# Performance work log

Hardware: AMD Instinct MI355X
Metric: run time of the kernel (lower is better)

## Reference

```python
import jax, jax.numpy as jnp
import numpy as np

N_NODES = 100000
N_EDGES = 600000
D_FEAT = 128
N_OUT = 1


def setup_inputs() -> dict:
    key = jax.random.key(0)
    k1, k2, k3, k4 = jax.random.split(key, 4)
    node_inputs = jax.random.normal(k1, (N_NODES, D_FEAT), dtype=jnp.float32)
    r_indices = jax.random.randint(k2, (N_EDGES,), 0, N_NODES, dtype=jnp.int64)
    c_indices = jax.random.randint(k3, (N_EDGES,), 0, N_NODES, dtype=jnp.int64)
    w = jax.random.normal(k4, (D_FEAT, N_OUT), dtype=jnp.float32) * 0.05
    b = jnp.zeros((N_OUT,), dtype=jnp.float32)
    return {"node_inputs": node_inputs, "r_indices": r_indices,
            "c_indices": c_indices, "w": w, "b": b}


def reference(node_inputs, r_indices, c_indices, w, b):
    # Gather edge endpoints: [E, D]
    row_inputs = node_inputs[r_indices]
    col_inputs = node_inputs[c_indices]
    diff = jnp.abs(row_inputs - col_inputs)          # [E, D]
    out = diff @ w + b                               # [E, n_out]
    out = jnp.squeeze(out, axis=-1)                  # n_out == 1
    return out  # act is identity (default)
```

## Files before the change

### kernel.cpp

```cpp
#include <hip/hip_runtime.h>
#include <hip/hip_bf16.h>


#define D_FEAT 128

__global__ __launch_bounds__(256) void mlp_decoder_edge_kernel(
    const float* __restrict__ nodes,
    const int*   __restrict__ r_idx,
    const int*   __restrict__ c_idx,
    const float* __restrict__ w,
    const float* __restrict__ b,
    float*       __restrict__ out,
    int n_edges)
{
    const int tid  = blockIdx.x * blockDim.x + threadIdx.x;
    const int lane = tid & 31;
    const int edge = tid >> 5;
    if (edge >= n_edges) return;

    const int r = r_idx[edge];
    const int c = c_idx[edge];

    const float4 wv = ((const float4*)w)[lane];

    const float4 av = ((const float4*)(nodes + (size_t)r * D_FEAT))[lane];
    const float4 bv = ((const float4*)(nodes + (size_t)c * D_FEAT))[lane];

    float s = fabsf(av.x - bv.x) * wv.x
            + fabsf(av.y - bv.y) * wv.y
            + fabsf(av.z - bv.z) * wv.z
            + fabsf(av.w - bv.w) * wv.w;

    #pragma unroll
    for (int off = 16; off > 0; off >>= 1)
        s += __shfl_xor(s, off, 64);

    if (lane == 0)
        out[edge] = s + b[0];
}

extern "C" void kernel_launch(void* const* d_in, const int* in_sizes, int n_in,
                              void* d_out, int out_size, void* d_ws, size_t ws_size,
                              hipStream_t stream) {
    const float* nodes = (const float*)d_in[0];
    const int*   r_idx = (const int*)d_in[1];
    const int*   c_idx = (const int*)d_in[2];
    const float* w     = (const float*)d_in[3];
    const float* b     = (const float*)d_in[4];
    float*       out   = (float*)d_out;

    const int n_edges = in_sizes[1];
    const int threads_needed = n_edges * 32;
    const int block = 256;
    const int grid  = (threads_needed + block - 1) / block;

    mlp_decoder_edge_kernel<<<grid, block, 0, stream>>>(
        nodes, r_idx, c_idx, w, b, out, n_edges);
}
```

Before: 159.6 us.

## Convert node table to fp16 in a pre-pass and gather half-precision rows

Adds a kernel that converts the fp32 node feature table into an fp16 copy in workspace on every call. A new edge kernel then gathers fp16 rows using 16 lanes per edge, eight features per lane, accumulating in fp32. The aim is to halve the bytes moved by the random row gathers, which dominate the cost. In exchange it pays for an extra full-table read and write plus a second launch, and rounding inputs to fp16 adds error. The original fp32 path is kept as a fallback when the workspace is too small.

```diff
diff --git a/kernel.cpp b/kernel.cpp
--- a/kernel.cpp
+++ b/kernel.cpp
@@ -1,10 +1,74 @@
 #include <hip/hip_runtime.h>
 #include <hip/hip_bf16.h>
+#include <hip/hip_fp16.h>
 
 
 #define D_FEAT 128
 
-__global__ __launch_bounds__(256) void mlp_decoder_edge_kernel(
+__global__ __launch_bounds__(256) void convert_f32_to_f16(
+    const float* __restrict__ src, __half* __restrict__ dst, int n8)
+{
+    const int i = blockIdx.x * blockDim.x + threadIdx.x;
+    if (i >= n8) return;
+    const float4* s = (const float4*)src + 2 * (size_t)i;
+    const float4 a = s[0];
+    const float4 c = s[1];
+    float4 packed;
+    ((__half2*)&packed)[0] = __floats2half2_rn(a.x, a.y);
+    ((__half2*)&packed)[1] = __floats2half2_rn(a.z, a.w);
+    ((__half2*)&packed)[2] = __floats2half2_rn(c.x, c.y);
+    ((__half2*)&packed)[3] = __floats2half2_rn(c.z, c.w);
+    ((float4*)dst)[i] = packed;
+}
+
+__global__ __launch_bounds__(256) void gather_edges_f16(
+    const __half* __restrict__ tbl,
+    const int*   __restrict__ r_idx,
+    const int*   __restrict__ c_idx,
+    const float* __restrict__ w,
+    const float* __restrict__ b,
+    float*       __restrict__ out,
+    int n_edges)
+{
+    const int tid  = blockIdx.x * blockDim.x + threadIdx.x;
+    const int lane = tid & 15;
+    const int edge = tid >> 4;
+    if (edge >= n_edges) return;
+
+    const int r = r_idx[edge];
+    const int c = c_idx[edge];
+
+    const float4 w0 = ((const float4*)w)[2 * lane + 0];
+    const float4 w1 = ((const float4*)w)[2 * lane + 1];
+
+    const float4 araw = ((const float4*)(tbl + (size_t)r * D_FEAT))[lane];
+    const float4 braw = ((const float4*)(tbl + (size_t)c * D_FEAT))[lane];
+    const __half2* ah = (const __half2*)&araw;
+    const __half2* bh = (const __half2*)&braw;
+
+    const float2 a0 = __half22float2(ah[0]), b0 = __half22float2(bh[0]);
+    const float2 a1 = __half22float2(ah[1]), b1 = __half22float2(bh[1]);
+    const float2 a2 = __half22float2(ah[2]), b2 = __half22float2(bh[2]);
+    const float2 a3 = __half22float2(ah[3]), b3 = __half22float2(bh[3]);
+
+    float s = fabsf(a0.x - b0.x) * w0.x
+            + fabsf(a0.y - b0.y) * w0.y
+            + fabsf(a1.x - b1.x) * w0.z
+            + fabsf(a1.y - b1.y) * w0.w
+            + fabsf(a2.x - b2.x) * w1.x
+            + fabsf(a2.y - b2.y) * w1.y
+            + fabsf(a3.x - b3.x) * w1.z
+            + fabsf(a3.y - b3.y) * w1.w;
+
+    #pragma unroll
+    for (int off = 8; off > 0; off >>= 1)
+        s += __shfl_xor(s, off, 64);
+
+    if (lane == 0)
+        out[edge] = s + b[0];
+}
+
+__global__ __launch_bounds__(256) void gather_edges_f32(
     const float* __restrict__ nodes,
     const int*   __restrict__ r_idx,
     const int*   __restrict__ c_idx,
@@ -22,7 +86,6 @@
     const int c = c_idx[edge];
 
     const float4 wv = ((const float4*)w)[lane];
-
     const float4 av = ((const float4*)(nodes + (size_t)r * D_FEAT))[lane];
     const float4 bv = ((const float4*)(nodes + (size_t)c * D_FEAT))[lane];
 
@@ -49,11 +112,26 @@
     const float* b     = (const float*)d_in[4];
     float*       out   = (float*)d_out;
 
-    const int n_edges = in_sizes[1];
-    const int threads_needed = n_edges * 32;
-    const int block = 256;
-    const int grid  = (threads_needed + block - 1) / block;
+    const int n_edges   = in_sizes[1];
+    const int n_nodes_f = in_sizes[0];
+    const size_t tbl_bytes = (size_t)n_nodes_f * sizeof(__half);
 
-    mlp_decoder_edge_kernel<<<grid, block, 0, stream>>>(
-        nodes, r_idx, c_idx, w, b, out, n_edges);
+    if (ws_size >= tbl_bytes && (n_nodes_f & 7) == 0) {
+        __half* tbl = (__half*)d_ws;
+
+        const int n8 = n_nodes_f / 8;
+        const int cblock = 256;
+        const int cgrid  = (n8 + cblock - 1) / cblock;
+        convert_f32_to_f16<<<cgrid, cblock, 0, stream>>>(nodes, tbl, n8);
+
+        const int block = 256;
+        const int grid  = (n_edges * 16 + block - 1) / block;
+        gather_edges_f16<<<grid, block, 0, stream>>>(
+            tbl, r_idx, c_idx, w, b, out, n_edges);
+    } else {
+        const int block = 256;
+        const int grid  = (n_edges * 32 + block - 1) / block;
+        gather_edges_f32<<<grid, block, 0, stream>>>(
+            nodes, r_idx, c_idx, w, b, out, n_edges);
+    }
 }
```

Result: faster. 131.1 us (-17.9%).
